# Kernel tuning notes

Hardware: AMD Instinct MI355X
Metric: run time of the kernel (lower is better)

## Reference

```python
import jax, jax.numpy as jnp
import numpy as np

N_QUBITS = 10
N_LAYERS = 4
DIM = 2 ** N_QUBITS  # 1024 statevector entries

# Z-expectation sign table: signs[d, q] = +1 if bit q of basis state d is 0 else -1
_bits = (np.arange(DIM)[:, None] >> (N_QUBITS - 1 - np.arange(N_QUBITS))) & 1
Z_SIGNS = jnp.asarray(1.0 - 2.0 * _bits, dtype=jnp.float32)  # [DIM, N_QUBITS]


def _apply_1q(state, mat, q):
    """Apply a 2x2 gate on qubit q. state: [B, DIM]; mat: [2,2] or [B,2,2]."""
    left, right = 2 ** q, 2 ** (N_QUBITS - q - 1)
    s = state.reshape(-1, left, 2, right)
    if mat.ndim == 3:
        s = jnp.einsum('bij,bljr->blir', mat, s)
    else:
        s = jnp.einsum('ij,bljr->blir', mat, s)
    return s.reshape(-1, DIM)


def _cnot_adj(state, q):
    """CNOT with control q, target q+1 (adjacent wires)."""
    left, right = 2 ** q, 2 ** (N_QUBITS - q - 2)
    s = state.reshape(-1, left, 2, 2, right)
    s = jnp.stack([s[:, :, 0], s[:, :, 1, ::-1]], axis=2)  # flip target where control=1
    return s.reshape(-1, DIM)


def _cnot_wrap(state):
    """CNOT with control = last qubit, target = qubit 0 (ring closure)."""
    s = state.reshape(-1, 2, 2 ** (N_QUBITS - 2), 2)  # [B, target, mid, control]
    s = jnp.stack([s[..., 0], s[:, ::-1, :, 1]], axis=-1)
    return s.reshape(-1, DIM)


def _circuit(x, weights):
    B = x.shape[0]
    state = jnp.zeros((B, DIM), jnp.complex64).at[:, 0].set(1.0)  # |0...0>

    # RX angle embedding (batch-dependent gates)
    c = jnp.cos(0.5 * x).astype(jnp.complex64)           # [B, n]
    s = (-1j) * jnp.sin(0.5 * x).astype(jnp.complex64)   # [B, n]
    for q in range(N_QUBITS):
        mat = jnp.stack([jnp.stack([c[:, q], s[:, q]], -1),
                         jnp.stack([s[:, q], c[:, q]], -1)], -2)  # [B,2,2]
        state = _apply_1q(state, mat, q)

    # BasicEntanglerLayers: per-qubit RY (shared weights) + CNOT ring
    w = weights.reshape(N_LAYERS, N_QUBITS)
    ch = jnp.cos(0.5 * w).astype(jnp.complex64)
    sh = jnp.sin(0.5 * w).astype(jnp.complex64)
    for l in range(N_LAYERS):
        for q in range(N_QUBITS):
            mat = jnp.stack([jnp.stack([ch[l, q], -sh[l, q]], -1),
                             jnp.stack([sh[l, q], ch[l, q]], -1)], -2)  # [2,2]
            state = _apply_1q(state, mat, q)
        for q in range(N_QUBITS - 1):
            state = _cnot_adj(state, q)
        state = _cnot_wrap(state)

    probs = state.real ** 2 + state.imag ** 2  # [B, DIM]
    return probs @ Z_SIGNS                     # [B, N_QUBITS] PauliZ expectations


def setup_inputs() -> dict:
    key = jax.random.key(0)
    k1, k2 = jax.random.split(key)
    x = jax.random.normal(k1, (2048, N_QUBITS), dtype=jnp.float32)
    weights = jax.random.normal(k2, (N_LAYERS * N_QUBITS,), dtype=jnp.float32)
    return {"x": x, "weights": weights}


def reference(x, weights):
    # Equivalent of: torch.stack([qnode(x[i], weights) for i in range(B)])
    # but fully batched over the statevector.
    return _circuit(x, weights)
```

## Files before the change

### kernel.cpp

```cpp
#include <hip/hip_runtime.h>

#define NQ 10


typedef float v2f __attribute__((ext_vector_type(2)));

template<int CTRL>
__device__ __forceinline__ float dppf(float v) {
    const int i = __float_as_int(v);
    const int r = __builtin_amdgcn_update_dpp(i, i, CTRL, 0xF, 0xF, false);
    return __int_as_float(r);
}
template<int OFF>
__device__ __forceinline__ float swzf(float v) {
    return __int_as_float(__builtin_amdgcn_ds_swizzle(__float_as_int(v), OFF));
}
__device__ __forceinline__ float bpermf(int addr4, float v) {
    return __int_as_float(__builtin_amdgcn_ds_bpermute(addr4, __float_as_int(v)));
}
__device__ __forceinline__ float rdlane(float v, int l) {
    return __int_as_float(__builtin_amdgcn_readlane(__float_as_int(v), l));
}
__device__ __forceinline__ v2f splat(float a) { v2f r; r.x = a; r.y = a; return r; }
__device__ __forceinline__ v2f cmul(v2f a, v2f b) {
    v2f r;
    r.x = a.x * b.x - a.y * b.y;
    r.y = a.x * b.y + a.y * b.x;
    return r;
}

__global__ __launch_bounds__(256) void qnn_kernel(const float* __restrict__ x,
                                                  const float* __restrict__ w,
                                                  float* __restrict__ out,
                                                  int B) {
    const int lane = threadIdx.x & 63;
    const int b = blockIdx.x * 4 + (threadIdx.x >> 6);
    if (b >= B) return;

    float cxv = 1.f, sxv = 0.f, cwv = 1.f, swv = 0.f;
    if (lane < NQ) {
        const float a = 0.5f * x[b * NQ + lane];
        cxv = cosf(a); sxv = sinf(a);
    }
    if (lane < 4 * NQ) {
        const float a = 0.5f * w[lane];
        cwv = cosf(a); swv = sinf(a);
    }

    v2f u0[NQ], u1[NQ];
#pragma unroll
    for (int q = 0; q < NQ; ++q) {
        const float c  = rdlane(cxv, q), s  = rdlane(sxv, q);
        const float ch = rdlane(cwv, q), sh = rdlane(swv, q);
        u0[q].x = ch * c;  u0[q].y = sh * s;
        u1[q].x = sh * c;  u1[q].y = -ch * s;
    }

    v2f ml = (lane & 1) ? u1[9] : u0[9];
#pragma unroll
    for (int p = 1; p < 6; ++p) {
        const v2f f = ((lane >> p) & 1) ? u1[9 - p] : u0[9 - p];
        ml = cmul(ml, f);
    }
    v2f m01[4], m23[4], tml[4];
#pragma unroll
    for (int j = 0; j < 4; ++j) {
        m01[j] = cmul((j & 1) ? u1[3] : u0[3], (j & 2) ? u1[2] : u0[2]);
        m23[j] = cmul((j & 1) ? u1[1] : u0[1], (j & 2) ? u1[0] : u0[0]);
    }
#pragma unroll
    for (int j = 0; j < 4; ++j) tml[j] = cmul(ml, m01[j]);

    v2f v[16];
#pragma unroll
    for (int r = 0; r < 16; ++r) v[r] = cmul(tml[r & 3], m23[r >> 2]);

    int t = lane;
    t ^= ((t >> 1) & 1) << 0;
    t ^= ((t >> 2) & 1) << 1;
    t ^= ((t >> 3) & 1) << 2;
    t ^= ((t >> 4) & 1) << 3;
    t ^= ((t >> 5) & 1) << 4;
    const int ga4 = t << 2;
    const int gb4 = (t ^ 32) << 2;
    const int a32 = (lane ^ 32) << 2;
    const bool wrapctl = (lane & 1);

#pragma unroll
    for (int l = 0; l < 3; ++l) {
        { v2f tmp;
          tmp = v[8];  v[8]  = v[12]; v[12] = tmp;
          tmp = v[9];  v[9]  = v[13]; v[13] = tmp;
          tmp = v[10]; v[10] = v[14]; v[14] = tmp;
          tmp = v[11]; v[11] = v[15]; v[15] = tmp; }
        { v2f tmp;
          tmp = v[4];  v[4]  = v[6];  v[6]  = tmp;
          tmp = v[5];  v[5]  = v[7];  v[7]  = tmp;
          tmp = v[12]; v[12] = v[14]; v[14] = tmp;
          tmp = v[13]; v[13] = v[15]; v[15] = tmp; }
        { v2f tmp;
          tmp = v[2];  v[2]  = v[3];  v[3]  = tmp;
          tmp = v[6];  v[6]  = v[7];  v[7]  = tmp;
          tmp = v[10]; v[10] = v[11]; v[11] = tmp;
          tmp = v[14]; v[14] = v[15]; v[15] = tmp; }
#pragma unroll
        for (int r = 0; r < 16; ++r) {
            const int a4 = (r & 1) ? gb4 : ga4;
            v[r].x = bpermf(a4, v[r].x);
            v[r].y = bpermf(a4, v[r].y);
        }
#pragma unroll
        for (int r = 0; r < 8; ++r) {
            const v2f a = v[r], c2 = v[r + 8];
            v[r]     = wrapctl ? c2 : a;
            v[r + 8] = wrapctl ? a : c2;
        }

        const int base = (l + 1) * NQ;
#pragma unroll
        for (int q = 0; q < 4; ++q) {
            const v2f C = splat(rdlane(cwv, base + q));
            const v2f S = splat(rdlane(swv, base + q));
            const int m = 1 << (3 - q);
#pragma unroll
            for (int r = 0; r < 16; ++r) {
                if (!(r & m)) {
                    const int r1 = r | m;
                    const v2f a0 = v[r], a1 = v[r1];
                    v[r]  = C * a0 - S * a1;
                    v[r1] = S * a0 + C * a1;
                }
            }
        }
        {
            const float c = rdlane(cwv, base + 4);
            const float s = rdlane(swv, base + 4);
            const v2f C = splat(c);
            const v2f SS = splat((lane & 32) ? s : -s);
#pragma unroll
            for (int r = 0; r < 16; ++r) {
                v2f o; o.x = bpermf(a32, v[r].x); o.y = bpermf(a32, v[r].y);
                v[r] = C * v[r] + SS * o;
            }
        }
        {
            const float c = rdlane(cwv, base + 5);
            const float s = rdlane(swv, base + 5);
            const v2f C = splat(c);
            const v2f SS = splat((lane & 16) ? s : -s);
#pragma unroll
            for (int r = 0; r < 16; ++r) {
                v2f o; o.x = swzf<0x401F>(v[r].x); o.y = swzf<0x401F>(v[r].y);
                v[r] = C * v[r] + SS * o;
            }
        }
        {
            const float c = rdlane(cwv, base + 6);
            const float s = rdlane(swv, base + 6);
            const v2f C = splat(c);
            const v2f SS = splat((lane & 8) ? s : -s);
#pragma unroll
            for (int r = 0; r < 16; ++r) {
                v2f o; o.x = dppf<0x128>(v[r].x); o.y = dppf<0x128>(v[r].y);
                v[r] = C * v[r] + SS * o;
            }
        }
        {
            const float c = rdlane(cwv, base + 7);
            const float s = rdlane(swv, base + 7);
            const v2f C = splat(c);
            const v2f SS = splat((lane & 4) ? s : -s);
#pragma unroll
            for (int r = 0; r < 16; ++r) {
                v2f o; o.x = swzf<0x101F>(v[r].x); o.y = swzf<0x101F>(v[r].y);
                v[r] = C * v[r] + SS * o;
            }
        }
        {
            const float c = rdlane(cwv, base + 8);
            const float s = rdlane(swv, base + 8);
            const v2f C = splat(c);
            const v2f SS = splat((lane & 2) ? s : -s);
#pragma unroll
            for (int r = 0; r < 16; ++r) {
                v2f o; o.x = dppf<0x4E>(v[r].x); o.y = dppf<0x4E>(v[r].y);
                v[r] = C * v[r] + SS * o;
            }
        }
        {
            const float c = rdlane(cwv, base + 9);
            const float s = rdlane(swv, base + 9);
            const v2f C = splat(c);
            const v2f SS = splat((lane & 1) ? s : -s);
#pragma unroll
            for (int r = 0; r < 16; ++r) {
                v2f o; o.x = dppf<0xB1>(v[r].x); o.y = dppf<0xB1>(v[r].y);
                v[r] = C * v[r] + SS * o;
            }
        }
    }

    float p[16];
#pragma unroll
    for (int r = 0; r < 16; ++r) p[r] = v[r].x * v[r].x + v[r].y * v[r].y;

    float S15 = 0.f, S7 = 0.f, S12 = 0.f, S14 = 0.f;
#pragma unroll
    for (int r = 0; r < 16; ++r) {
        const float pr = p[r];
        S15 += (__popc(r) & 1)      ? -pr : pr;
        S7  += (__popc(r & 7) & 1)  ? -pr : pr;
        S12 += (__popc(r & 12) & 1) ? -pr : pr;
        S14 += (__popc(r & 14) & 1) ? -pr : pr;
    }

    const float gAll = (__popc(lane) & 1) ? -1.f : 1.f;
    float acc[NQ];
    acc[0] = gAll * S7;
    acc[1] = S12;
    acc[2] = S14;
    acc[3] = S15;
    acc[4] = ((lane >> 5) & 1) ? -S15 : S15;
    acc[5] = (__popc(lane & 0x30) & 1) ? -S15 : S15;
    acc[6] = (__popc(lane & 0x38) & 1) ? -S15 : S15;
    acc[7] = (__popc(lane & 0x3C) & 1) ? -S15 : S15;
    acc[8] = (__popc(lane & 0x3E) & 1) ? -S15 : S15;
    acc[9] = gAll * S15;

#pragma unroll
    for (int q = 0; q < NQ; ++q) {
        float a = acc[q];
        a += bpermf(a32, a);
        a += swzf<0x401F>(a);
        a += dppf<0x128>(a);
        a += swzf<0x101F>(a);
        a += dppf<0x4E>(a);
        a += dppf<0xB1>(a);
        acc[q] = a;
    }
    if (lane == 0) {
#pragma unroll
        for (int q = 0; q < NQ; ++q) out[b * NQ + q] = acc[q];
    }
}

extern "C" void kernel_launch(void* const* d_in, const int* in_sizes, int n_in,
                              void* d_out, int out_size, void* d_ws, size_t ws_size,
                              hipStream_t stream) {
    const float* x = (const float*)d_in[0];
    const float* w = (const float*)d_in[1];
    float* out = (float*)d_out;
    const int B = in_sizes[0] / NQ;
    qnn_kernel<<<(B + 3) / 4, 256, 0, stream>>>(x, w, out, B);
}
```

Before: 66.75 us.

## Split each sample's statevector across two waves with LDS exchange

Each batch sample now runs on a 128-thread block of two wavefronts, and each lane holds 8 amplitudes instead of 16. The gate on qubit 0 pairs amplitudes held by different waves, so it is done through a double-buffered shared-memory exchange with __syncthreads. The final Z-expectation partial sums are combined across the two waves through shared memory. This halves per-thread register use and doubles thread-level parallelism, at the cost of extra LDS traffic and block-wide barriers in each layer.

```diff
diff --git a/kernel.cpp b/kernel.cpp
--- a/kernel.cpp
+++ b/kernel.cpp
@@ -29,13 +29,17 @@
     return r;
 }
 
-__global__ __launch_bounds__(256) void qnn_kernel(const float* __restrict__ x,
+__global__ __launch_bounds__(128) void qnn_kernel(const float* __restrict__ x,
                                                   const float* __restrict__ w,
                                                   float* __restrict__ out,
                                                   int B) {
-    const int lane = threadIdx.x & 63;
-    const int b = blockIdx.x * 4 + (threadIdx.x >> 6);
-    if (b >= B) return;
+    const int tid  = threadIdx.x;
+    const int lane = tid & 63;
+    const int wv   = tid >> 6;
+    const int b    = blockIdx.x;
+
+    __shared__ v2f  xch[2][2][8][64];
+    __shared__ float red[NQ];
 
     float cxv = 1.f, sxv = 0.f, cwv = 1.f, swv = 0.f;
     if (lane < NQ) {
@@ -62,18 +66,16 @@
         const v2f f = ((lane >> p) & 1) ? u1[9 - p] : u0[9 - p];
         ml = cmul(ml, f);
     }
-    v2f m01[4], m23[4], tml[4];
+    const v2f f0 = wv ? u1[0] : u0[0];
+    v2f t01[2] = { cmul(f0, u0[1]), cmul(f0, u1[1]) };
+    v2f m01[4];
 #pragma unroll
     for (int j = 0; j < 4; ++j) {
         m01[j] = cmul((j & 1) ? u1[3] : u0[3], (j & 2) ? u1[2] : u0[2]);
-        m23[j] = cmul((j & 1) ? u1[1] : u0[1], (j & 2) ? u1[0] : u0[0]);
-    }
-#pragma unroll
-    for (int j = 0; j < 4; ++j) tml[j] = cmul(ml, m01[j]);
-
-    v2f v[16];
-#pragma unroll
-    for (int r = 0; r < 16; ++r) v[r] = cmul(tml[r & 3], m23[r >> 2]);
+    }
+    v2f v[8];
+#pragma unroll
+    for (int j = 0; j < 8; ++j) v[j] = cmul(cmul(ml, t01[j >> 2]), m01[j & 3]);
 
     int t = lane;
     t ^= ((t >> 1) & 1) << 0;
@@ -84,51 +86,59 @@
     const int ga4 = t << 2;
     const int gb4 = (t ^ 32) << 2;
     const int a32 = (lane ^ 32) << 2;
-    const bool wrapctl = (lane & 1);
+    const bool odd = (lane & 1);
 
 #pragma unroll
     for (int l = 0; l < 3; ++l) {
+        if (wv) {
+            v2f tmp;
+            tmp = v[0]; v[0] = v[4]; v[4] = tmp;
+            tmp = v[1]; v[1] = v[5]; v[5] = tmp;
+            tmp = v[2]; v[2] = v[6]; v[6] = tmp;
+            tmp = v[3]; v[3] = v[7]; v[7] = tmp;
+        }
         { v2f tmp;
-          tmp = v[8];  v[8]  = v[12]; v[12] = tmp;
-          tmp = v[9];  v[9]  = v[13]; v[13] = tmp;
-          tmp = v[10]; v[10] = v[14]; v[14] = tmp;
-          tmp = v[11]; v[11] = v[15]; v[15] = tmp; }
+          tmp = v[4]; v[4] = v[6]; v[6] = tmp;
+          tmp = v[5]; v[5] = v[7]; v[7] = tmp; }
         { v2f tmp;
-          tmp = v[4];  v[4]  = v[6];  v[6]  = tmp;
-          tmp = v[5];  v[5]  = v[7];  v[7]  = tmp;
-          tmp = v[12]; v[12] = v[14]; v[14] = tmp;
-          tmp = v[13]; v[13] = v[15]; v[15] = tmp; }
-        { v2f tmp;
-          tmp = v[2];  v[2]  = v[3];  v[3]  = tmp;
-          tmp = v[6];  v[6]  = v[7];  v[7]  = tmp;
-          tmp = v[10]; v[10] = v[11]; v[11] = tmp;
-          tmp = v[14]; v[14] = v[15]; v[15] = tmp; }
-#pragma unroll
-        for (int r = 0; r < 16; ++r) {
-            const int a4 = (r & 1) ? gb4 : ga4;
-            v[r].x = bpermf(a4, v[r].x);
-            v[r].y = bpermf(a4, v[r].y);
-        }
-#pragma unroll
-        for (int r = 0; r < 8; ++r) {
-            const v2f a = v[r], c2 = v[r + 8];
-            v[r]     = wrapctl ? c2 : a;
-            v[r + 8] = wrapctl ? a : c2;
-        }
-
+          tmp = v[2]; v[2] = v[3]; v[3] = tmp;
+          tmp = v[6]; v[6] = v[7]; v[7] = tmp; }
+#pragma unroll
+        for (int j = 0; j < 8; ++j) {
+            const int a4 = (j & 1) ? gb4 : ga4;
+            v[j].x = bpermf(a4, v[j].x);
+            v[j].y = bpermf(a4, v[j].y);
+        }
         const int base = (l + 1) * NQ;
-#pragma unroll
-        for (int q = 0; q < 4; ++q) {
+        const int buf = l & 1;
+#pragma unroll
+        for (int j = 0; j < 8; ++j) xch[buf][wv][j][lane] = v[j];
+        __syncthreads();
+        {
+            const float c = rdlane(cwv, base + 0);
+            const float s = rdlane(swv, base + 0);
+            const v2f C = splat(c);
+            const v2f S = splat(wv ? s : -s);
+#pragma unroll
+            for (int j = 0; j < 8; ++j) {
+                const v2f u2 = xch[buf][wv ^ 1][j][lane];
+                const v2f mine = odd ? u2 : v[j];
+                const v2f part = odd ? v[j] : u2;
+                v[j] = C * mine + S * part;
+            }
+        }
+#pragma unroll
+        for (int q = 1; q < 4; ++q) {
             const v2f C = splat(rdlane(cwv, base + q));
             const v2f S = splat(rdlane(swv, base + q));
             const int m = 1 << (3 - q);
 #pragma unroll
-            for (int r = 0; r < 16; ++r) {
-                if (!(r & m)) {
-                    const int r1 = r | m;
-                    const v2f a0 = v[r], a1 = v[r1];
-                    v[r]  = C * a0 - S * a1;
-                    v[r1] = S * a0 + C * a1;
+            for (int j = 0; j < 8; ++j) {
+                if (!(j & m)) {
+                    const int j1 = j | m;
+                    const v2f a0 = v[j], a1 = v[j1];
+                    v[j]  = C * a0 - S * a1;
+                    v[j1] = S * a0 + C * a1;
                 }
             }
         }
@@ -138,9 +148,9 @@
             const v2f C = splat(c);
             const v2f SS = splat((lane & 32) ? s : -s);
 #pragma unroll
-            for (int r = 0; r < 16; ++r) {
-                v2f o; o.x = bpermf(a32, v[r].x); o.y = bpermf(a32, v[r].y);
-                v[r] = C * v[r] + SS * o;
+            for (int j = 0; j < 8; ++j) {
+                v2f o; o.x = bpermf(a32, v[j].x); o.y = bpermf(a32, v[j].y);
+                v[j] = C * v[j] + SS * o;
             }
         }
         {
@@ -149,9 +159,9 @@
             const v2f C = splat(c);
             const v2f SS = splat((lane & 16) ? s : -s);
 #pragma unroll
-            for (int r = 0; r < 16; ++r) {
-                v2f o; o.x = swzf<0x401F>(v[r].x); o.y = swzf<0x401F>(v[r].y);
-                v[r] = C * v[r] + SS * o;
+            for (int j = 0; j < 8; ++j) {
+                v2f o; o.x = swzf<0x401F>(v[j].x); o.y = swzf<0x401F>(v[j].y);
+                v[j] = C * v[j] + SS * o;
             }
         }
         {
@@ -160,9 +170,9 @@
             const v2f C = splat(c);
             const v2f SS = splat((lane & 8) ? s : -s);
 #pragma unroll
-            for (int r = 0; r < 16; ++r) {
-                v2f o; o.x = dppf<0x128>(v[r].x); o.y = dppf<0x128>(v[r].y);
-                v[r] = C * v[r] + SS * o;
+            for (int j = 0; j < 8; ++j) {
+                v2f o; o.x = dppf<0x128>(v[j].x); o.y = dppf<0x128>(v[j].y);
+                v[j] = C * v[j] + SS * o;
             }
         }
         {
@@ -171,9 +181,9 @@
             const v2f C = splat(c);
             const v2f SS = splat((lane & 4) ? s : -s);
 #pragma unroll
-            for (int r = 0; r < 16; ++r) {
-                v2f o; o.x = swzf<0x101F>(v[r].x); o.y = swzf<0x101F>(v[r].y);
-                v[r] = C * v[r] + SS * o;
+            for (int j = 0; j < 8; ++j) {
+                v2f o; o.x = swzf<0x101F>(v[j].x); o.y = swzf<0x101F>(v[j].y);
+                v[j] = C * v[j] + SS * o;
             }
         }
         {
@@ -182,9 +192,9 @@
             const v2f C = splat(c);
             const v2f SS = splat((lane & 2) ? s : -s);
 #pragma unroll
-            for (int r = 0; r < 16; ++r) {
-                v2f o; o.x = dppf<0x4E>(v[r].x); o.y = dppf<0x4E>(v[r].y);
-                v[r] = C * v[r] + SS * o;
+            for (int j = 0; j < 8; ++j) {
+                v2f o; o.x = dppf<0x4E>(v[j].x); o.y = dppf<0x4E>(v[j].y);
+                v[j] = C * v[j] + SS * o;
             }
         }
         {
@@ -193,39 +203,35 @@
             const v2f C = splat(c);
             const v2f SS = splat((lane & 1) ? s : -s);
 #pragma unroll
-            for (int r = 0; r < 16; ++r) {
-                v2f o; o.x = dppf<0xB1>(v[r].x); o.y = dppf<0xB1>(v[r].y);
-                v[r] = C * v[r] + SS * o;
-            }
-        }
-    }
-
-    float p[16];
-#pragma unroll
-    for (int r = 0; r < 16; ++r) p[r] = v[r].x * v[r].x + v[r].y * v[r].y;
-
-    float S15 = 0.f, S7 = 0.f, S12 = 0.f, S14 = 0.f;
-#pragma unroll
-    for (int r = 0; r < 16; ++r) {
-        const float pr = p[r];
-        S15 += (__popc(r) & 1)      ? -pr : pr;
-        S7  += (__popc(r & 7) & 1)  ? -pr : pr;
-        S12 += (__popc(r & 12) & 1) ? -pr : pr;
-        S14 += (__popc(r & 14) & 1) ? -pr : pr;
-    }
-
+            for (int j = 0; j < 8; ++j) {
+                v2f o; o.x = dppf<0xB1>(v[j].x); o.y = dppf<0xB1>(v[j].y);
+                v[j] = C * v[j] + SS * o;
+            }
+        }
+    }
+
+    float T7 = 0.f, T4 = 0.f, T6 = 0.f;
+#pragma unroll
+    for (int j = 0; j < 8; ++j) {
+        const float pj = v[j].x * v[j].x + v[j].y * v[j].y;
+        T7 += (__popc(j) & 1)     ? -pj : pj;
+        T4 += (j & 4)             ? -pj : pj;
+        T6 += (__popc(j & 6) & 1) ? -pj : pj;
+    }
+    const float sw   = wv ? -1.f : 1.f;
     const float gAll = (__popc(lane) & 1) ? -1.f : 1.f;
+    const float W7 = sw * T7;
     float acc[NQ];
-    acc[0] = gAll * S7;
-    acc[1] = S12;
-    acc[2] = S14;
-    acc[3] = S15;
-    acc[4] = ((lane >> 5) & 1) ? -S15 : S15;
-    acc[5] = (__popc(lane & 0x30) & 1) ? -S15 : S15;
-    acc[6] = (__popc(lane & 0x38) & 1) ? -S15 : S15;
-    acc[7] = (__popc(lane & 0x3C) & 1) ? -S15 : S15;
-    acc[8] = (__popc(lane & 0x3E) & 1) ? -S15 : S15;
-    acc[9] = gAll * S15;
+    acc[0] = gAll * T7;
+    acc[1] = sw * T4;
+    acc[2] = sw * T6;
+    acc[3] = W7;
+    acc[4] = ((lane >> 5) & 1) ? -W7 : W7;
+    acc[5] = (__popc(lane & 0x30) & 1) ? -W7 : W7;
+    acc[6] = (__popc(lane & 0x38) & 1) ? -W7 : W7;
+    acc[7] = (__popc(lane & 0x3C) & 1) ? -W7 : W7;
+    acc[8] = (__popc(lane & 0x3E) & 1) ? -W7 : W7;
+    acc[9] = gAll * W7;
 
 #pragma unroll
     for (int q = 0; q < NQ; ++q) {
@@ -238,9 +244,14 @@
         a += dppf<0xB1>(a);
         acc[q] = a;
     }
-    if (lane == 0) {
-#pragma unroll
-        for (int q = 0; q < NQ; ++q) out[b * NQ + q] = acc[q];
+    if (wv == 1 && lane == 0) {
+#pragma unroll
+        for (int q = 0; q < NQ; ++q) red[q] = acc[q];
+    }
+    __syncthreads();
+    if (wv == 0 && lane == 0) {
+#pragma unroll
+        for (int q = 0; q < NQ; ++q) out[b * NQ + q] = acc[q] + red[q];
     }
 }
 
@@ -251,5 +262,5 @@
     const float* w = (const float*)d_in[1];
     float* out = (float*)d_out;
     const int B = in_sizes[0] / NQ;
-    qnn_kernel<<<(B + 3) / 4, 256, 0, stream>>>(x, w, out, B);
-}
+    qnn_kernel<<<B, 128, 0, stream>>>(x, w, out, B);
+}
```

Result: no change. 68.05 us (+1.9%).

## Process two batch samples per wavefront and replace swizzles with DPP in reductions

Applied to the files above, without the earlier changes.

Each wavefront now simulates two statevectors, with 32 complex registers per lane, so the weight trig setup and launch overhead are shared and the interleaved independent shuffles give more instruction-level parallelism. The xor-4 swizzle is replaced by a pair of DPP row ops. The final cross-lane reduction drops its bpermute and swizzle steps in favour of DPP plus four readlanes. Register pressure roughly doubles, and the layer loop is no longer unrolled, so occupancy may drop. B=2048 gives only 1024 waves, so fewer of the GPU's compute units get work.

```diff
diff --git a/kernel.cpp b/kernel.cpp
--- a/kernel.cpp
+++ b/kernel.cpp
@@ -20,6 +20,9 @@
 }
 __device__ __forceinline__ float rdlane(float v, int l) {
     return __int_as_float(__builtin_amdgcn_readlane(__float_as_int(v), l));
+}
+__device__ __forceinline__ float xor4f(float v) {
+    return dppf<0x1B>(dppf<0x141>(v));
 }
 __device__ __forceinline__ v2f splat(float a) { v2f r; r.x = a; r.y = a; return r; }
 __device__ __forceinline__ v2f cmul(v2f a, v2f b) {
@@ -34,46 +37,53 @@
                                                   float* __restrict__ out,
                                                   int B) {
     const int lane = threadIdx.x & 63;
-    const int b = blockIdx.x * 4 + (threadIdx.x >> 6);
-    if (b >= B) return;
-
-    float cxv = 1.f, sxv = 0.f, cwv = 1.f, swv = 0.f;
-    if (lane < NQ) {
-        const float a = 0.5f * x[b * NQ + lane];
-        cxv = cosf(a); sxv = sinf(a);
-    }
+    const int wid  = blockIdx.x * 4 + (threadIdx.x >> 6);
+    const int b0   = wid * 2;
+    if (b0 >= B) return;
+
+    float cwv = 1.f, swv = 0.f;
     if (lane < 4 * NQ) {
         const float a = 0.5f * w[lane];
         cwv = cosf(a); swv = sinf(a);
     }
-
-    v2f u0[NQ], u1[NQ];
-#pragma unroll
-    for (int q = 0; q < NQ; ++q) {
-        const float c  = rdlane(cxv, q), s  = rdlane(sxv, q);
-        const float ch = rdlane(cwv, q), sh = rdlane(swv, q);
-        u0[q].x = ch * c;  u0[q].y = sh * s;
-        u1[q].x = sh * c;  u1[q].y = -ch * s;
-    }
-
-    v2f ml = (lane & 1) ? u1[9] : u0[9];
-#pragma unroll
-    for (int p = 1; p < 6; ++p) {
-        const v2f f = ((lane >> p) & 1) ? u1[9 - p] : u0[9 - p];
-        ml = cmul(ml, f);
-    }
-    v2f m01[4], m23[4], tml[4];
-#pragma unroll
-    for (int j = 0; j < 4; ++j) {
-        m01[j] = cmul((j & 1) ? u1[3] : u0[3], (j & 2) ? u1[2] : u0[2]);
-        m23[j] = cmul((j & 1) ? u1[1] : u0[1], (j & 2) ? u1[0] : u0[0]);
-    }
-#pragma unroll
-    for (int j = 0; j < 4; ++j) tml[j] = cmul(ml, m01[j]);
-
-    v2f v[16];
-#pragma unroll
-    for (int r = 0; r < 16; ++r) v[r] = cmul(tml[r & 3], m23[r >> 2]);
+    float cxA = 1.f, sxA = 0.f, cxB = 1.f, sxB = 0.f;
+    if (lane < NQ) {
+        const float a0 = 0.5f * x[b0 * NQ + lane];
+        cxA = cosf(a0); sxA = sinf(a0);
+        const float a1 = 0.5f * x[(b0 + 1) * NQ + lane];
+        cxB = cosf(a1); sxB = sinf(a1);
+    }
+
+    v2f v[32];
+#pragma unroll
+    for (int s = 0; s < 2; ++s) {
+        const float cxv = s ? cxB : cxA;
+        const float sxv = s ? sxB : sxA;
+        v2f u0[NQ], u1[NQ];
+#pragma unroll
+        for (int q = 0; q < NQ; ++q) {
+            const float c  = rdlane(cxv, q), si = rdlane(sxv, q);
+            const float ch = rdlane(cwv, q), sh = rdlane(swv, q);
+            u0[q].x = ch * c;  u0[q].y = sh * si;
+            u1[q].x = sh * c;  u1[q].y = -ch * si;
+        }
+        v2f ml = (lane & 1) ? u1[9] : u0[9];
+#pragma unroll
+        for (int p = 1; p < 6; ++p) {
+            const v2f f = ((lane >> p) & 1) ? u1[9 - p] : u0[9 - p];
+            ml = cmul(ml, f);
+        }
+        v2f m01[4], m23[4], tml[4];
+#pragma unroll
+        for (int j = 0; j < 4; ++j) {
+            m01[j] = cmul((j & 1) ? u1[3] : u0[3], (j & 2) ? u1[2] : u0[2]);
+            m23[j] = cmul((j & 1) ? u1[1] : u0[1], (j & 2) ? u1[0] : u0[0]);
+        }
+#pragma unroll
+        for (int j = 0; j < 4; ++j) tml[j] = cmul(ml, m01[j]);
+#pragma unroll
+        for (int r = 0; r < 16; ++r) v[s * 16 + r] = cmul(tml[r & 3], m23[r >> 2]);
+    }
 
     int t = lane;
     t ^= ((t >> 1) & 1) << 0;
@@ -86,34 +96,38 @@
     const int a32 = (lane ^ 32) << 2;
     const bool wrapctl = (lane & 1);
 
-#pragma unroll
+#pragma unroll 1
     for (int l = 0; l < 3; ++l) {
-        { v2f tmp;
-          tmp = v[8];  v[8]  = v[12]; v[12] = tmp;
-          tmp = v[9];  v[9]  = v[13]; v[13] = tmp;
-          tmp = v[10]; v[10] = v[14]; v[14] = tmp;
-          tmp = v[11]; v[11] = v[15]; v[15] = tmp; }
-        { v2f tmp;
-          tmp = v[4];  v[4]  = v[6];  v[6]  = tmp;
-          tmp = v[5];  v[5]  = v[7];  v[7]  = tmp;
-          tmp = v[12]; v[12] = v[14]; v[14] = tmp;
-          tmp = v[13]; v[13] = v[15]; v[15] = tmp; }
-        { v2f tmp;
-          tmp = v[2];  v[2]  = v[3];  v[3]  = tmp;
-          tmp = v[6];  v[6]  = v[7];  v[7]  = tmp;
-          tmp = v[10]; v[10] = v[11]; v[11] = tmp;
-          tmp = v[14]; v[14] = v[15]; v[15] = tmp; }
-#pragma unroll
-        for (int r = 0; r < 16; ++r) {
+#pragma unroll
+        for (int h = 0; h < 32; h += 16) {
+            v2f tmp;
+            tmp = v[h+8];  v[h+8]  = v[h+12]; v[h+12] = tmp;
+            tmp = v[h+9];  v[h+9]  = v[h+13]; v[h+13] = tmp;
+            tmp = v[h+10]; v[h+10] = v[h+14]; v[h+14] = tmp;
+            tmp = v[h+11]; v[h+11] = v[h+15]; v[h+15] = tmp;
+            tmp = v[h+4];  v[h+4]  = v[h+6];  v[h+6]  = tmp;
+            tmp = v[h+5];  v[h+5]  = v[h+7];  v[h+7]  = tmp;
+            tmp = v[h+12]; v[h+12] = v[h+14]; v[h+14] = tmp;
+            tmp = v[h+13]; v[h+13] = v[h+15]; v[h+15] = tmp;
+            tmp = v[h+2];  v[h+2]  = v[h+3];  v[h+3]  = tmp;
+            tmp = v[h+6];  v[h+6]  = v[h+7];  v[h+7]  = tmp;
+            tmp = v[h+10]; v[h+10] = v[h+11]; v[h+11] = tmp;
+            tmp = v[h+14]; v[h+14] = v[h+15]; v[h+15] = tmp;
+        }
+#pragma unroll
+        for (int r = 0; r < 32; ++r) {
             const int a4 = (r & 1) ? gb4 : ga4;
             v[r].x = bpermf(a4, v[r].x);
             v[r].y = bpermf(a4, v[r].y);
         }
 #pragma unroll
-        for (int r = 0; r < 8; ++r) {
-            const v2f a = v[r], c2 = v[r + 8];
-            v[r]     = wrapctl ? c2 : a;
-            v[r + 8] = wrapctl ? a : c2;
+        for (int h = 0; h < 32; h += 16) {
+#pragma unroll
+            for (int r = 0; r < 8; ++r) {
+                const v2f a = v[h + r], c2 = v[h + r + 8];
+                v[h + r]     = wrapctl ? c2 : a;
+                v[h + r + 8] = wrapctl ? a : c2;
+            }
         }
 
         const int base = (l + 1) * NQ;
@@ -123,7 +137,7 @@
             const v2f S = splat(rdlane(swv, base + q));
             const int m = 1 << (3 - q);
 #pragma unroll
-            for (int r = 0; r < 16; ++r) {
+            for (int r = 0; r < 32; ++r) {
                 if (!(r & m)) {
                     const int r1 = r | m;
                     const v2f a0 = v[r], a1 = v[r1];
@@ -138,7 +152,7 @@
             const v2f C = splat(c);
             const v2f SS = splat((lane & 32) ? s : -s);
 #pragma unroll
-            for (int r = 0; r < 16; ++r) {
+            for (int r = 0; r < 32; ++r) {
                 v2f o; o.x = bpermf(a32, v[r].x); o.y = bpermf(a32, v[r].y);
                 v[r] = C * v[r] + SS * o;
             }
@@ -149,7 +163,7 @@
             const v2f C = splat(c);
             const v2f SS = splat((lane & 16) ? s : -s);
 #pragma unroll
-            for (int r = 0; r < 16; ++r) {
+            for (int r = 0; r < 32; ++r) {
                 v2f o; o.x = swzf<0x401F>(v[r].x); o.y = swzf<0x401F>(v[r].y);
                 v[r] = C * v[r] + SS * o;
             }
@@ -160,7 +174,7 @@
             const v2f C = splat(c);
             const v2f SS = splat((lane & 8) ? s : -s);
 #pragma unroll
-            for (int r = 0; r < 16; ++r) {
+            for (int r = 0; r < 32; ++r) {
                 v2f o; o.x = dppf<0x128>(v[r].x); o.y = dppf<0x128>(v[r].y);
                 v[r] = C * v[r] + SS * o;
             }
@@ -171,8 +185,8 @@
             const v2f C = splat(c);
             const v2f SS = splat((lane & 4) ? s : -s);
 #pragma unroll
-            for (int r = 0; r < 16; ++r) {
-                v2f o; o.x = swzf<0x101F>(v[r].x); o.y = swzf<0x101F>(v[r].y);
+            for (int r = 0; r < 32; ++r) {
+                v2f o; o.x = xor4f(v[r].x); o.y = xor4f(v[r].y);
                 v[r] = C * v[r] + SS * o;
             }
         }
@@ -182,7 +196,7 @@
             const v2f C = splat(c);
             const v2f SS = splat((lane & 2) ? s : -s);
 #pragma unroll
-            for (int r = 0; r < 16; ++r) {
+            for (int r = 0; r < 32; ++r) {
                 v2f o; o.x = dppf<0x4E>(v[r].x); o.y = dppf<0x4E>(v[r].y);
                 v[r] = C * v[r] + SS * o;
             }
@@ -193,54 +207,51 @@
             const v2f C = splat(c);
             const v2f SS = splat((lane & 1) ? s : -s);
 #pragma unroll
-            for (int r = 0; r < 16; ++r) {
+            for (int r = 0; r < 32; ++r) {
                 v2f o; o.x = dppf<0xB1>(v[r].x); o.y = dppf<0xB1>(v[r].y);
                 v[r] = C * v[r] + SS * o;
             }
         }
     }
 
-    float p[16];
-#pragma unroll
-    for (int r = 0; r < 16; ++r) p[r] = v[r].x * v[r].x + v[r].y * v[r].y;
-
-    float S15 = 0.f, S7 = 0.f, S12 = 0.f, S14 = 0.f;
-#pragma unroll
-    for (int r = 0; r < 16; ++r) {
-        const float pr = p[r];
-        S15 += (__popc(r) & 1)      ? -pr : pr;
-        S7  += (__popc(r & 7) & 1)  ? -pr : pr;
-        S12 += (__popc(r & 12) & 1) ? -pr : pr;
-        S14 += (__popc(r & 14) & 1) ? -pr : pr;
-    }
-
     const float gAll = (__popc(lane) & 1) ? -1.f : 1.f;
-    float acc[NQ];
-    acc[0] = gAll * S7;
-    acc[1] = S12;
-    acc[2] = S14;
-    acc[3] = S15;
-    acc[4] = ((lane >> 5) & 1) ? -S15 : S15;
-    acc[5] = (__popc(lane & 0x30) & 1) ? -S15 : S15;
-    acc[6] = (__popc(lane & 0x38) & 1) ? -S15 : S15;
-    acc[7] = (__popc(lane & 0x3C) & 1) ? -S15 : S15;
-    acc[8] = (__popc(lane & 0x3E) & 1) ? -S15 : S15;
-    acc[9] = gAll * S15;
-
-#pragma unroll
-    for (int q = 0; q < NQ; ++q) {
-        float a = acc[q];
-        a += bpermf(a32, a);
-        a += swzf<0x401F>(a);
-        a += dppf<0x128>(a);
-        a += swzf<0x101F>(a);
-        a += dppf<0x4E>(a);
-        a += dppf<0xB1>(a);
-        acc[q] = a;
-    }
-    if (lane == 0) {
-#pragma unroll
-        for (int q = 0; q < NQ; ++q) out[b * NQ + q] = acc[q];
+#pragma unroll
+    for (int s = 0; s < 2; ++s) {
+        float S15 = 0.f, S7 = 0.f, S12 = 0.f, S14 = 0.f;
+#pragma unroll
+        for (int r = 0; r < 16; ++r) {
+            const v2f a = v[s * 16 + r];
+            const float pr = a.x * a.x + a.y * a.y;
+            S15 += (__popc(r) & 1)      ? -pr : pr;
+            S7  += (__popc(r & 7) & 1)  ? -pr : pr;
+            S12 += (__popc(r & 12) & 1) ? -pr : pr;
+            S14 += (__popc(r & 14) & 1) ? -pr : pr;
+        }
+        float acc[NQ];
+        acc[0] = gAll * S7;
+        acc[1] = S12;
+        acc[2] = S14;
+        acc[3] = S15;
+        acc[4] = ((lane >> 5) & 1) ? -S15 : S15;
+        acc[5] = (__popc(lane & 0x30) & 1) ? -S15 : S15;
+        acc[6] = (__popc(lane & 0x38) & 1) ? -S15 : S15;
+        acc[7] = (__popc(lane & 0x3C) & 1) ? -S15 : S15;
+        acc[8] = (__popc(lane & 0x3E) & 1) ? -S15 : S15;
+        acc[9] = gAll * S15;
+
+#pragma unroll
+        for (int q = 0; q < NQ; ++q) {
+            float a = acc[q];
+            a += dppf<0x128>(a);
+            a += xor4f(a);
+            a += dppf<0x4E>(a);
+            a += dppf<0xB1>(a);
+            acc[q] = rdlane(a, 0) + rdlane(a, 16) + rdlane(a, 32) + rdlane(a, 48);
+        }
+        if (lane == 0) {
+#pragma unroll
+            for (int q = 0; q < NQ; ++q) out[(b0 + s) * NQ + q] = acc[q];
+        }
     }
 }
 
@@ -251,5 +262,6 @@
     const float* w = (const float*)d_in[1];
     float* out = (float*)d_out;
     const int B = in_sizes[0] / NQ;
-    qnn_kernel<<<(B + 3) / 4, 256, 0, stream>>>(x, w, out, B);
-}
+    const int waves = (B + 1) / 2;
+    qnn_kernel<<<(waves + 3) / 4, 256, 0, stream>>>(x, w, out, B);
+}
```

After: 69.93 us. 4.8% more time.
